# Kernel optimization log

Hardware: AMD Instinct MI355X
Metric: run time of the kernel (lower is better)

Reference implementation:

```python
import jax, jax.numpy as jnp
import numpy as np

D = 768      # hidden_size
H = 12       # num_head
HD = D // H  # head_dim
LN_EPS = 1e-5


def setup_inputs() -> dict:
    key = jax.random.key(0)
    ks = jax.random.split(key, 9)
    N, S = 4, 2048
    s = 0.02
    return {
        "hidden_state": jax.random.normal(ks[0], (N, S, D), dtype=jnp.float32),
        "key_padding_mask": jax.random.randint(ks[1], (N, S), 0, 2, dtype=jnp.int64),
        "Wq": jax.random.normal(ks[2], (D, D), dtype=jnp.float32) * s,
        "Wk": jax.random.normal(ks[3], (D, D), dtype=jnp.float32) * s,
        "Wv": jax.random.normal(ks[4], (D, D), dtype=jnp.float32) * s,
        "Wo": jax.random.normal(ks[5], (D, D), dtype=jnp.float32) * s,
        "W1": jax.random.normal(ks[6], (4 * D, D), dtype=jnp.float32) * s,
        "W2": jax.random.normal(ks[7], (D, 4 * D), dtype=jnp.float32) * s,
        "ln_g": jnp.ones((D,), dtype=jnp.float32),
        "ln_b": jnp.zeros((D,), dtype=jnp.float32),
    }


def _layernorm(x, g, b):
    mu = jnp.mean(x, axis=-1, keepdims=True)
    var = jnp.mean(jnp.square(x - mu), axis=-1, keepdims=True)
    return (x - mu) * jax.lax.rsqrt(var + LN_EPS) * g + b


def reference(hidden_state, key_padding_mask, Wq, Wk, Wv, Wo, W1, W2, ln_g, ln_b):
    x = hidden_state
    N, S, _ = x.shape
    # Note: original module projects K and V from `query` (self-attention).
    def proj(W):
        return (x @ W.T).reshape(N, S, H, HD).transpose(0, 2, 1, 3)  # [N,H,S,HD]
    Q, K, V = proj(Wq), proj(Wk), proj(Wv)
    scores = jnp.einsum("bhqd,bhkd->bhqk", Q, K)  # [N,H,S,S]
    # int mask: 0 marks padding positions -> masked with -inf
    pad = (key_padding_mask == 0)[:, None, None, :]  # [N,1,1,S]
    scores = jnp.where(pad, -jnp.inf, scores)
    attn = jax.nn.softmax(scores / np.sqrt(HD), axis=-1)
    ctx = jnp.einsum("bhqk,bhkd->bhqd", attn, V)
    ctx = ctx.transpose(0, 2, 1, 3).reshape(N, S, D)
    mha = ctx @ Wo.T
    # residual + LayerNorm (same LN params used twice, as in the original)
    n1 = _layernorm(x + mha, ln_g, ln_b)
    # FFN with exact GELU (torch nn.GELU default)
    f = jax.nn.gelu(n1 @ W1.T, approximate=False) @ W2.T
    return _layernorm(n1 + f, ln_g, ln_b)
```

## Files before the change

kernel.cpp:

```cpp
#include <hip/hip_runtime.h>
#include <math.h>

typedef unsigned short u16;
typedef unsigned int u32;
typedef __bf16 bf16x8 __attribute__((ext_vector_type(8)));
typedef float f32x4 __attribute__((ext_vector_type(4)));
typedef u32 u32x4 __attribute__((ext_vector_type(4)));

#define NB 4
#define SS 2048
#define DD 768
#define HH 12
#define HD 64
#define ROWS (NB*SS)

__device__ __forceinline__ u16 f2bf(float f) {
    union { float f; unsigned u; } v; v.f = f;
    unsigned r = v.u + 0x7fffu + ((v.u >> 16) & 1u);
    return (u16)(r >> 16);
}
__device__ __forceinline__ u32 fas(float f) { union { float f; u32 u; } v; v.f = f; return v.u; }

__device__ __forceinline__ void gl_lds16(const void* g, void* l) {
    __builtin_amdgcn_global_load_lds((__attribute__((address_space(1))) void*)(g),
                                     (__attribute__((address_space(3))) void*)(l),
                                     16, 0, 0);
}

__global__ __launch_bounds__(256) void prep_kernel(
        const float* __restrict__ X, const float* __restrict__ Wq,
        const float* __restrict__ Wk, const float* __restrict__ Wv,
        const float* __restrict__ Wo, const float* __restrict__ W1,
        const float* __restrict__ W2, const int* __restrict__ mask,
        u16* __restrict__ Xb, u16* __restrict__ Wqkvb, u16* __restrict__ Wob,
        u16* __restrict__ W1b, u16* __restrict__ W2b,
        int* __restrict__ cidx, int* __restrict__ cnt) {
    const int blk = blockIdx.x, tid = threadIdx.x;
    const float* src; u16* dst; int idx;
    if (blk < 6144)       { src = X;  dst = Xb;               idx = blk * 1024 + tid * 4; }
    else if (blk < 6720)  { src = Wq; dst = Wqkvb;            idx = (blk - 6144) * 1024 + tid * 4; }
    else if (blk < 7296)  { src = Wk; dst = Wqkvb + DD * DD;  idx = (blk - 6720) * 1024 + tid * 4; }
    else if (blk < 7872)  { src = Wv; dst = Wqkvb + 2*DD*DD;  idx = (blk - 7296) * 1024 + tid * 4; }
    else if (blk < 8448)  { src = Wo; dst = Wob;              idx = (blk - 7872) * 1024 + tid * 4; }
    else if (blk < 10752) { src = W1; dst = W1b;              idx = (blk - 8448) * 1024 + tid * 4; }
    else if (blk < 13056) { src = W2; dst = W2b;              idx = (blk - 10752) * 1024 + tid * 4; }
    else {
        const int b = blk - 13056;
        const int lane = tid & 63, wave = tid >> 6;
        const int base = b * SS + tid * 8;
        int4 m0 = *(const int4*)&mask[base];
        int4 m1 = *(const int4*)&mask[base + 4];
        int v[8] = { m0.x != 0, m0.y != 0, m0.z != 0, m0.w != 0,
                     m1.x != 0, m1.y != 0, m1.z != 0, m1.w != 0 };
        int own = 0;
#pragma unroll
        for (int i = 0; i < 8; ++i) own += v[i];
        int inc = own;
#pragma unroll
        for (int o = 1; o < 64; o <<= 1) {
            int n = __shfl_up(inc, o);
            if (lane >= o) inc += n;
        }
        __shared__ int wsum[4];
        if (lane == 63) wsum[wave] = inc;
        __syncthreads();
        int wbase = 0;
#pragma unroll
        for (int w = 0; w < 4; ++w) wbase += (w < wave) ? wsum[w] : 0;
        int pos = wbase + inc - own;
        int o8[8];
#pragma unroll
        for (int i = 0; i < 8; ++i) { o8[i] = v[i] ? pos : -1; pos += v[i]; }
        *(int4*)&cidx[base]     = make_int4(o8[0], o8[1], o8[2], o8[3]);
        *(int4*)&cidx[base + 4] = make_int4(o8[4], o8[5], o8[6], o8[7]);
        if (tid == 255) cnt[b] = wbase + inc;
        return;
    }
    float4 v = *(const float4*)&src[idx];
    ushort4 o;
    o.x = f2bf(v.x); o.y = f2bf(v.y); o.z = f2bf(v.z); o.w = f2bf(v.w);
    *(ushort4*)&dst[idx] = o;
}

template <int EPI, int BN>
__global__ __launch_bounds__(256) void gemm_bt(const u16* __restrict__ A,
                                               const u16* __restrict__ B,
                                               int M, int N, int K,
                                               void* __restrict__ out,
                                               const void* __restrict__ aux,
                                               u16* __restrict__ Qb,
                                               u16* __restrict__ Kb,
                                               u16* __restrict__ Vb,
                                               const int* __restrict__ cidx) {
    __shared__ __align__(16) u16 lA[2][128 * 64];
    __shared__ __align__(16) u16 lB[2][BN * 64];
    constexpr int MI = (BN == 128) ? 4 : 2;
    const int tid = threadIdx.x;
    const int lane = tid & 63, wave = tid >> 6;
    const int quad = lane >> 4, lc = lane & 15;
    const int xcd = blockIdx.x & 7, loc = blockIdx.x >> 3;
    const int mb = xcd * 8 + (loc & 7), nb = loc >> 3;
    const int m0 = mb * 128, n0 = nb * BN;
    const int wrow = (BN == 128) ? (wave >> 1) * 64 : wave * 32;
    const int wcol = (BN == 128) ? (wave & 1) * 64 : 0;
    const int swz = lc & 7;

    auto stage = [&](int bi, int kb) {
#pragma unroll
        for (int p0 = 0; p0 < 1024; p0 += 256) {
            int p = p0 + tid, row = p >> 3, cl = (p & 7) ^ (row & 7);
            gl_lds16(A + (size_t)(m0 + row) * K + kb + cl * 8, &lA[bi][(size_t)(p0 + wave * 64) * 8]);
        }
#pragma unroll
        for (int p0 = 0; p0 < BN * 8; p0 += 256) {
            int p = p0 + tid, row = p >> 3, cl = (p & 7) ^ (row & 7);
            gl_lds16(B + (size_t)(n0 + row) * K + kb + cl * 8, &lB[bi][(size_t)(p0 + wave * 64) * 8]);
        }
    };

    f32x4 acc[MI][4] = {};
    const int KT = K >> 6;

    stage(0, 0);
    for (int t = 0; t < KT; ++t) {
        const int cur = t & 1;
        if (t < KT - 1) {
            stage(cur ^ 1, (t + 1) << 6);
            __builtin_amdgcn_sched_barrier(0);
            if constexpr (BN == 128) asm volatile("s_waitcnt vmcnt(8)" ::: "memory");
            else                     asm volatile("s_waitcnt vmcnt(6)" ::: "memory");
        } else {
            __builtin_amdgcn_sched_barrier(0);
            asm volatile("s_waitcnt vmcnt(0)" ::: "memory");
        }
        __builtin_amdgcn_sched_barrier(0);
        __builtin_amdgcn_s_barrier();
        __builtin_amdgcn_sched_barrier(0);

        const u16* bA = &lA[cur][0];
        const u16* bB = &lB[cur][0];
#pragma unroll
        for (int k2 = 0; k2 < 2; ++k2) {
            bf16x8 af[MI], bfr[4];
#pragma unroll
            for (int t_ = 0; t_ < MI; ++t_)
                af[t_] = *(const bf16x8*)&bA[(wrow + t_ * 16 + lc) * 64 + ((quad + k2 * 4) ^ swz) * 8];
#pragma unroll
            for (int t_ = 0; t_ < 4; ++t_)
                bfr[t_] = *(const bf16x8*)&bB[(wcol + t_ * 16 + lc) * 64 + ((quad + k2 * 4) ^ swz) * 8];
            __builtin_amdgcn_s_setprio(1);
#pragma unroll
            for (int mi = 0; mi < MI; ++mi)
#pragma unroll
                for (int ni = 0; ni < 4; ++ni)
                    acc[mi][ni] = __builtin_amdgcn_mfma_f32_16x16x32_bf16(af[mi], bfr[ni],
                                                                         acc[mi][ni], 0, 0, 0);
            __builtin_amdgcn_s_setprio(0);
        }
        __builtin_amdgcn_sched_barrier(0);
        __builtin_amdgcn_s_barrier();
    }

#pragma unroll
    for (int mi = 0; mi < MI; ++mi) {
        int csa[4];
        if constexpr (EPI == 0) {
            int mbase = m0 + wrow + mi * 16 + quad * 4;
            int4 cs4 = *(const int4*)&cidx[(mbase >> 11) * SS + (mbase & 2047)];
            csa[0] = cs4.x; csa[1] = cs4.y; csa[2] = cs4.z; csa[3] = cs4.w;
        }
#pragma unroll
        for (int r = 0; r < 4; ++r) {
            int m = m0 + wrow + mi * 16 + quad * 4 + r;
#pragma unroll
            for (int ni = 0; ni < 4; ++ni) {
                int n = n0 + wcol + ni * 16 + lc;
                float v = acc[mi][ni][r];
                if constexpr (EPI == 0) {
                    int b = m >> 11, s = m & 2047;
                    int which = n / DD, rem = n - which * DD;
                    int h = rem >> 6, d = rem & 63;
                    u16* dst = which == 0 ? Qb : (which == 1 ? Kb : Vb);
                    int sidx = which == 0 ? s : csa[r];
                    if (sidx >= 0)
                        dst[((((size_t)b * HH + h) * SS + sidx) << 6) + d] = f2bf(v);
                } else if constexpr (EPI == 1) {
                    float u = v * fmaf(v * v, 0.035677408f, 0.7978845608f);
                    float e = __builtin_amdgcn_exp2f(u * 2.885390082f);
                    float g = v - v * __builtin_amdgcn_rcpf(e + 1.0f);
                    ((u16*)out)[(size_t)m * N + n] = f2bf(g);
                } else if constexpr (EPI == 2) {
                    ((float*)out)[(size_t)m * N + n] =
                        v + ((const float*)aux)[(size_t)m * N + n];
                } else {
                    ((float*)out)[(size_t)m * N + n] =
                        v + (float)(((const __bf16*)aux)[(size_t)m * N + n]);
                }
            }
        }
    }
}

__global__ __launch_bounds__(256) void transpose_v(const u16* __restrict__ V,
                                                   u16* __restrict__ Vt,
                                                   const int* __restrict__ cnt) {
    __shared__ u16 t[32][33];
    int bh = blockIdx.z;
    int c = cnt[bh / HH];
    int cr = (c + 63) & ~63;
    int s0 = blockIdx.x * 32, d0 = blockIdx.y * 32;
    if (s0 >= cr) return;
    const u16* vb = V + (size_t)bh * SS * HD;
    u16* vtb = Vt + (size_t)bh * HD * SS;
    int tx = threadIdx.x & 31, ty = threadIdx.x >> 5;
#pragma unroll
    for (int i = 0; i < 32; i += 8) {
        int s = s0 + ty + i;
        t[ty + i][tx] = (s < c) ? vb[(size_t)s * HD + d0 + tx] : (u16)0;
    }
    __syncthreads();
#pragma unroll
    for (int i = 0; i < 32; i += 8) vtb[(size_t)(d0 + ty + i) * SS + s0 + tx] = t[tx][ty + i];
}

__global__ __launch_bounds__(256, 3) void attn_kernel(const u16* __restrict__ Q,
                                                      const u16* __restrict__ K,
                                                      const u16* __restrict__ Vt,
                                                      const int* __restrict__ cntg,
                                                      u16* __restrict__ Ctx) {
    __shared__ __align__(16) u16 lK[2][4096];
    __shared__ __align__(16) u16 lV[2][4096];
    const int tid = threadIdx.x, lane = tid & 63, wave = tid >> 6;
    const int quad = lane >> 4, lc = lane & 15;
    const int bh = blockIdx.x % (NB * HH);
    const int b = bh / HH, h = bh - b * HH;
    const int q0 = (blockIdx.x / (NB * HH)) * 128;
    const u16* Qg = Q + ((size_t)bh * SS + q0 + wave * 32) * HD;
    const u16* Kg = K + (size_t)bh * SS * HD;
    const u16* Vg = Vt + (size_t)bh * HD * SS;
    const int sw = lc & 7;
    const int cnt = cntg[b];
    const int nt = (cnt + 63) >> 6;

    const int srow = tid >> 3, scl = (tid & 7) ^ (srow & 7);
    const int srow2 = (256 + tid) >> 3, scl2 = (tid & 7) ^ (srow2 & 7);

    auto stage = [&](int bi, int j0) {
        gl_lds16(Kg + (size_t)(j0 + srow) * HD + scl * 8,   &lK[bi][(size_t)(wave * 64) * 8]);
        gl_lds16(Kg + (size_t)(j0 + srow2) * HD + scl2 * 8, &lK[bi][(size_t)(256 + wave * 64) * 8]);
        gl_lds16(Vg + (size_t)srow * SS + j0 + scl * 8,     &lV[bi][(size_t)(wave * 64) * 8]);
        gl_lds16(Vg + (size_t)srow2 * SS + j0 + scl2 * 8,   &lV[bi][(size_t)(256 + wave * 64) * 8]);
    };

    bf16x8 qf[2][2];
#pragma unroll
    for (int mi = 0; mi < 2; ++mi)
#pragma unroll
        for (int k2 = 0; k2 < 2; ++k2)
            qf[mi][k2] = *(const bf16x8*)(Qg + (size_t)(mi * 16 + lc) * HD + k2 * 32 + quad * 8);

    bf16x8 onesf;
#pragma unroll
    for (int i = 0; i < 8; ++i) onesf[i] = (__bf16)1.0f;

    f32x4 oacc[2][4] = {};
    f32x4 lsum[2] = {};

    stage(0, 0);
    for (int t = 0; t < nt; ++t) {
        const int cur = t & 1;
        if (t < nt - 1) {
            stage(cur ^ 1, (t + 1) * 64);
            __builtin_amdgcn_sched_barrier(0);
            asm volatile("s_waitcnt vmcnt(4)" ::: "memory");
        } else {
            __builtin_amdgcn_sched_barrier(0);
            asm volatile("s_waitcnt vmcnt(0)" ::: "memory");
        }
        __builtin_amdgcn_sched_barrier(0);
        __builtin_amdgcn_s_barrier();
        __builtin_amdgcn_sched_barrier(0);

        const u16* bK = &lK[cur][0];
        const u16* bV = &lV[cur][0];

        f32x4 sacc[2][4] = {};
        __builtin_amdgcn_s_setprio(1);
#pragma unroll
        for (int k2 = 0; k2 < 2; ++k2) {
            bf16x8 kf[4];
#pragma unroll
            for (int ni = 0; ni < 4; ++ni)
                kf[ni] = *(const bf16x8*)&bK[(ni * 16 + lc) * 64 + ((quad + k2 * 4) ^ sw) * 8];
#pragma unroll
            for (int ni = 0; ni < 4; ++ni) {
                sacc[0][ni] = __builtin_amdgcn_mfma_f32_16x16x32_bf16(kf[ni], qf[0][k2], sacc[0][ni], 0, 0, 0);
                sacc[1][ni] = __builtin_amdgcn_mfma_f32_16x16x32_bf16(kf[ni], qf[1][k2], sacc[1][ni], 0, 0, 0);
            }
        }
        __builtin_amdgcn_s_setprio(0);

        const int kb_ = cnt - t * 64;
        const bool part = kb_ < 64;
        u32 pa[2][4], pb[2][4];
#pragma unroll
        for (int ni = 0; ni < 4; ++ni) {
#pragma unroll
            for (int mi = 0; mi < 2; ++mi) {
#pragma unroll
                for (int r = 0; r < 4; ++r) {
                    float e = __builtin_amdgcn_exp2f(sacc[mi][ni][r] * 0.180336880f);
                    if (part) e = (ni * 16 + quad * 4 + r < kb_) ? e : 0.0f;
                    sacc[mi][ni][r] = e;
                }
                pa[mi][ni] = __builtin_amdgcn_perm(fas(sacc[mi][ni][1]), fas(sacc[mi][ni][0]), 0x07060302);
                pb[mi][ni] = __builtin_amdgcn_perm(fas(sacc[mi][ni][3]), fas(sacc[mi][ni][2]), 0x07060302);
            }
        }

        bf16x8 pf[2][2];
#pragma unroll
        for (int mi = 0; mi < 2; ++mi)
#pragma unroll
            for (int k2 = 0; k2 < 2; ++k2) {
                u32 xa = pa[mi][2 * k2], ya = pa[mi][2 * k2 + 1];
                u32 xb = pb[mi][2 * k2], yb = pb[mi][2 * k2 + 1];
                asm("v_permlane32_swap_b32 %0, %1" : "+v"(xa), "+v"(ya));
                asm("v_permlane16_swap_b32 %0, %1" : "+v"(xa), "+v"(ya));
                asm("v_permlane32_swap_b32 %0, %1" : "+v"(xb), "+v"(yb));
                asm("v_permlane16_swap_b32 %0, %1" : "+v"(xb), "+v"(yb));
                u32x4 pw = { xa, xb, ya, yb };
                pf[mi][k2] = __builtin_bit_cast(bf16x8, pw);
            }

        __builtin_amdgcn_s_setprio(1);
#pragma unroll
        for (int k2 = 0; k2 < 2; ++k2) {
            lsum[0] = __builtin_amdgcn_mfma_f32_16x16x32_bf16(pf[0][k2], onesf, lsum[0], 0, 0, 0);
            lsum[1] = __builtin_amdgcn_mfma_f32_16x16x32_bf16(pf[1][k2], onesf, lsum[1], 0, 0, 0);
#pragma unroll
            for (int ni = 0; ni < 4; ++ni) {
                bf16x8 vf = *(const bf16x8*)&bV[(ni * 16 + lc) * 64 + ((quad + k2 * 4) ^ sw) * 8];
                oacc[0][ni] = __builtin_amdgcn_mfma_f32_16x16x32_bf16(pf[0][k2], vf, oacc[0][ni], 0, 0, 0);
                oacc[1][ni] = __builtin_amdgcn_mfma_f32_16x16x32_bf16(pf[1][k2], vf, oacc[1][ni], 0, 0, 0);
            }
        }
        __builtin_amdgcn_s_setprio(0);

        __builtin_amdgcn_sched_barrier(0);
        __builtin_amdgcn_s_barrier();
    }

#pragma unroll
    for (int mi = 0; mi < 2; ++mi)
#pragma unroll
        for (int r = 0; r < 4; ++r) {
            float inv = 1.0f / lsum[mi][r];
            int s = q0 + wave * 32 + mi * 16 + quad * 4 + r;
            size_t base = ((size_t)(b * SS + s)) * DD + h * HD;
#pragma unroll
            for (int ni = 0; ni < 4; ++ni)
                Ctx[base + ni * 16 + lc] = f2bf(oacc[mi][ni][r] * inv);
        }
}

__global__ __launch_bounds__(256) void ln_kernel(const float* __restrict__ in,
                                                 const float* __restrict__ g,
                                                 const float* __restrict__ bb,
                                                 u16* __restrict__ out_bf,
                                                 float* __restrict__ out_f) {
    const int row = blockIdx.x, tid = threadIdx.x;
    const float* x = in + (size_t)row * DD;
    float v0 = x[tid], v1 = x[tid + 256], v2 = x[tid + 512];
    float s = v0 + v1 + v2;
    float q = v0 * v0 + v1 * v1 + v2 * v2;
#pragma unroll
    for (int o = 1; o < 64; o <<= 1) {
        s += __shfl_xor(s, o);
        q += __shfl_xor(q, o);
    }
    __shared__ float rs[4], rq[4];
    int wave = tid >> 6;
    if ((tid & 63) == 0) { rs[wave] = s; rq[wave] = q; }
    __syncthreads();
    s = rs[0] + rs[1] + rs[2] + rs[3];
    q = rq[0] + rq[1] + rq[2] + rq[3];
    float mu = s * (1.0f / DD);
    float var = q * (1.0f / DD) - mu * mu;
    float rstd = rsqrtf(var + 1e-5f);
#pragma unroll
    for (int j = 0; j < 3; ++j) {
        int col = tid + j * 256;
        float v = (j == 0 ? v0 : (j == 1 ? v1 : v2));
        float y = (v - mu) * rstd * g[col] + bb[col];
        if (out_bf) out_bf[(size_t)row * DD + col] = f2bf(y);
        if (out_f) out_f[(size_t)row * DD + col] = y;
    }
}

extern "C" void kernel_launch(void* const* d_in, const int* in_sizes, int n_in,
                              void* d_out, int out_size, void* d_ws, size_t ws_size,
                              hipStream_t stream) {
    const float* X    = (const float*)d_in[0];
    const int*   mask = (const int*)d_in[1];
    const float* Wq   = (const float*)d_in[2];
    const float* Wk   = (const float*)d_in[3];
    const float* Wv   = (const float*)d_in[4];
    const float* Wo   = (const float*)d_in[5];
    const float* W1   = (const float*)d_in[6];
    const float* W2   = (const float*)d_in[7];
    const float* ln_g = (const float*)d_in[8];
    const float* ln_b = (const float*)d_in[9];
    float* out = (float*)d_out;

    char* ws = (char*)d_ws;
    size_t off = 0;
    auto alloc = [&](size_t bytes) {
        void* p = ws + off;
        off += (bytes + 255) & ~(size_t)255;
        return p;
    };
    u16*   Xbf   = (u16*)alloc((size_t)ROWS * DD * 2);
    u16*   Wqkvb = (u16*)alloc((size_t)3 * DD * DD * 2);
    u16*   Wob   = (u16*)alloc((size_t)DD * DD * 2);
    u16*   W1b   = (u16*)alloc((size_t)4 * DD * DD * 2);
    u16*   W2b   = (u16*)alloc((size_t)4 * DD * DD * 2);
    int*   cidx  = (int*)alloc((size_t)NB * SS * 4);
    int*   cnt   = (int*)alloc(256);
    u16*   Qb    = (u16*)alloc((size_t)ROWS * DD * 2);
    u16*   Kb    = (u16*)alloc((size_t)ROWS * DD * 2);
    u16*   Vb    = (u16*)alloc((size_t)ROWS * DD * 2);
    u16*   Vtb   = (u16*)alloc((size_t)ROWS * DD * 2);
    float* resid = (float*)alloc((size_t)ROWS * DD * 4);
    u16*   n1b   = (u16*)alloc((size_t)ROWS * DD * 2);
    u16*   Gb    = Qb;
    u16*   Ctxb  = Xbf;
    float* h2    = resid;

    prep_kernel<<<dim3(13056 + NB), dim3(256), 0, stream>>>(
        X, Wq, Wk, Wv, Wo, W1, W2, mask,
        Xbf, Wqkvb, Wob, W1b, W2b, cidx, cnt);

    gemm_bt<0, 128><<<dim3((3 * DD / 128) * (ROWS / 128)), dim3(256), 0, stream>>>(
        Xbf, Wqkvb, ROWS, 3 * DD, DD, nullptr, nullptr, Qb, Kb, Vb, cidx);

    transpose_v<<<dim3(SS / 32, HD / 32, NB * HH), dim3(256), 0, stream>>>(Vb, Vtb, cnt);

    attn_kernel<<<dim3((SS / 128) * (NB * HH)), dim3(256), 0, stream>>>(
        Qb, Kb, Vtb, cnt, Ctxb);

    gemm_bt<2, 64><<<dim3((DD / 64) * (ROWS / 128)), dim3(256), 0, stream>>>(
        Ctxb, Wob, ROWS, DD, DD, resid, X, nullptr, nullptr, nullptr, nullptr);

    ln_kernel<<<dim3(ROWS), dim3(256), 0, stream>>>(resid, ln_g, ln_b, n1b, nullptr);

    gemm_bt<1, 128><<<dim3((4 * DD / 128) * (ROWS / 128)), dim3(256), 0, stream>>>(
        n1b, W1b, ROWS, 4 * DD, DD, Gb, nullptr, nullptr, nullptr, nullptr, nullptr);

    gemm_bt<3, 64><<<dim3((DD / 64) * (ROWS / 128)), dim3(256), 0, stream>>>(
        Gb, W2b, ROWS, DD, 4 * DD, h2, n1b, nullptr, nullptr, nullptr, nullptr);

    ln_kernel<<<dim3(ROWS), dim3(256), 0, stream>>>(h2, ln_g, ln_b, nullptr, out);
}
```

Before: 345.5 us.

## Add 256x256 eight-wave GEMM for FFN up-projection and simplify generic GEMM loop

Adds a new 512-thread GEMM kernel with 256x256 output tiles, double-buffered LDS and interleaved prefetch of A and B halves between MFMA phases, used for the W1 GEMM with the GELU epilogue. The larger tile raises arithmetic intensity and reuse of each staged tile. Separately, the generic gemm_bt kernel loses its double buffering and priority hints and becomes a single-buffer load/sync/compute loop, which likely exposes global load latency in the QKV, Wo and W2 GEMMs. The new kernel uses 128KB of LDS per block and a large accumulator count, which may limit occupancy.

```diff
diff --git a/kernel.cpp b/kernel.cpp
--- a/kernel.cpp
+++ b/kernel.cpp
@@ -92,8 +92,8 @@
                                                u16* __restrict__ Kb,
                                                u16* __restrict__ Vb,
                                                const int* __restrict__ cidx) {
-    __shared__ __align__(16) u16 lA[2][128 * 64];
-    __shared__ __align__(16) u16 lB[2][BN * 64];
+    __shared__ __align__(16) u16 lA[128 * 64];
+    __shared__ __align__(16) u16 lB[BN * 64];
     constexpr int MI = (BN == 128) ? 4 : 2;
     const int tid = threadIdx.x;
     const int lane = tid & 63, wave = tid >> 6;
@@ -105,60 +105,37 @@
     const int wcol = (BN == 128) ? (wave & 1) * 64 : 0;
     const int swz = lc & 7;
 
-    auto stage = [&](int bi, int kb) {
+    f32x4 acc[MI][4] = {};
+
+    for (int kb = 0; kb < K; kb += 64) {
+        __syncthreads();
 #pragma unroll
         for (int p0 = 0; p0 < 1024; p0 += 256) {
             int p = p0 + tid, row = p >> 3, cl = (p & 7) ^ (row & 7);
-            gl_lds16(A + (size_t)(m0 + row) * K + kb + cl * 8, &lA[bi][(size_t)(p0 + wave * 64) * 8]);
+            gl_lds16(A + (size_t)(m0 + row) * K + kb + cl * 8, &lA[(size_t)(p0 + wave * 64) * 8]);
         }
 #pragma unroll
         for (int p0 = 0; p0 < BN * 8; p0 += 256) {
             int p = p0 + tid, row = p >> 3, cl = (p & 7) ^ (row & 7);
-            gl_lds16(B + (size_t)(n0 + row) * K + kb + cl * 8, &lB[bi][(size_t)(p0 + wave * 64) * 8]);
-        }
-    };
-
-    f32x4 acc[MI][4] = {};
-    const int KT = K >> 6;
-
-    stage(0, 0);
-    for (int t = 0; t < KT; ++t) {
-        const int cur = t & 1;
-        if (t < KT - 1) {
-            stage(cur ^ 1, (t + 1) << 6);
-            __builtin_amdgcn_sched_barrier(0);
-            if constexpr (BN == 128) asm volatile("s_waitcnt vmcnt(8)" ::: "memory");
-            else                     asm volatile("s_waitcnt vmcnt(6)" ::: "memory");
-        } else {
-            __builtin_amdgcn_sched_barrier(0);
-            asm volatile("s_waitcnt vmcnt(0)" ::: "memory");
-        }
-        __builtin_amdgcn_sched_barrier(0);
-        __builtin_amdgcn_s_barrier();
-        __builtin_amdgcn_sched_barrier(0);
-
-        const u16* bA = &lA[cur][0];
-        const u16* bB = &lB[cur][0];
+            gl_lds16(B + (size_t)(n0 + row) * K + kb + cl * 8, &lB[(size_t)(p0 + wave * 64) * 8]);
+        }
+        __syncthreads();
 #pragma unroll
         for (int k2 = 0; k2 < 2; ++k2) {
             bf16x8 af[MI], bfr[4];
 #pragma unroll
-            for (int t_ = 0; t_ < MI; ++t_)
-                af[t_] = *(const bf16x8*)&bA[(wrow + t_ * 16 + lc) * 64 + ((quad + k2 * 4) ^ swz) * 8];
-#pragma unroll
-            for (int t_ = 0; t_ < 4; ++t_)
-                bfr[t_] = *(const bf16x8*)&bB[(wcol + t_ * 16 + lc) * 64 + ((quad + k2 * 4) ^ swz) * 8];
-            __builtin_amdgcn_s_setprio(1);
+            for (int t = 0; t < MI; ++t)
+                af[t] = *(const bf16x8*)&lA[(wrow + t * 16 + lc) * 64 + ((quad + k2 * 4) ^ swz) * 8];
+#pragma unroll
+            for (int t = 0; t < 4; ++t)
+                bfr[t] = *(const bf16x8*)&lB[(wcol + t * 16 + lc) * 64 + ((quad + k2 * 4) ^ swz) * 8];
 #pragma unroll
             for (int mi = 0; mi < MI; ++mi)
 #pragma unroll
                 for (int ni = 0; ni < 4; ++ni)
                     acc[mi][ni] = __builtin_amdgcn_mfma_f32_16x16x32_bf16(af[mi], bfr[ni],
                                                                          acc[mi][ni], 0, 0, 0);
-            __builtin_amdgcn_s_setprio(0);
-        }
-        __builtin_amdgcn_sched_barrier(0);
-        __builtin_amdgcn_s_barrier();
+        }
     }
 
 #pragma unroll
@@ -201,6 +178,158 @@
     }
 }
 
+template <int EPI>
+__global__ __launch_bounds__(512, 2) void gemm256_bt(const u16* __restrict__ A,
+                                                     const u16* __restrict__ B,
+                                                     int M, int N, int K,
+                                                     void* __restrict__ out) {
+    __shared__ __align__(16) u16 lA[2][256 * 64];
+    __shared__ __align__(16) u16 lB[2][256 * 64];
+    const int tid = threadIdx.x;
+    const int lane = tid & 63, wave = tid >> 6;
+    const int quad = lane >> 4, lc = lane & 15;
+    const int xcd = blockIdx.x & 7, loc = blockIdx.x >> 3;
+    const int mpx = (M >> 8) >> 3;
+    const int mb = xcd * mpx + (loc % mpx), nb = loc / mpx;
+    const int m0 = mb * 256, n0 = nb * 256;
+    const int wrow = (wave >> 2) * 128;
+    const int wcol = (wave & 3) * 64;
+    const int swz = lc & 7;
+
+    auto stageA = [&](int bi, int kb, int r) {
+        int p = r * 512 + tid, row = p >> 3, cl = (p & 7) ^ (row & 7);
+        gl_lds16(A + (size_t)(m0 + row) * K + kb + cl * 8,
+                 &lA[bi][(size_t)(r * 512 + wave * 64) * 8]);
+    };
+    auto stageB = [&](int bi, int kb, int r) {
+        int p = r * 512 + tid, row = p >> 3, cl = (p & 7) ^ (row & 7);
+        gl_lds16(B + (size_t)(n0 + row) * K + kb + cl * 8,
+                 &lB[bi][(size_t)(r * 512 + wave * 64) * 8]);
+    };
+
+    f32x4 acc[8][4] = {};
+    const int KT = K >> 6;
+
+#pragma unroll
+    for (int r = 0; r < 4; ++r) stageA(0, 0, r);
+#pragma unroll
+    for (int r = 0; r < 4; ++r) stageB(0, 0, r);
+    asm volatile("s_waitcnt vmcnt(0)" ::: "memory");
+    __builtin_amdgcn_sched_barrier(0);
+    __builtin_amdgcn_s_barrier();
+    __builtin_amdgcn_sched_barrier(0);
+
+    for (int t = 0; t < KT; ++t) {
+        const int cur = t & 1;
+        const u16* bA = &lA[cur][0];
+        const u16* bB = &lB[cur][0];
+        const bool pf = (t + 1) < KT;
+        const int kb1 = (t + 1) << 6;
+        bf16x8 af[4], bf[4];
+
+#pragma unroll
+        for (int i = 0; i < 4; ++i)
+            af[i] = *(const bf16x8*)&bA[(wrow + i * 16 + lc) * 64 + (quad ^ swz) * 8];
+#pragma unroll
+        for (int j = 0; j < 4; ++j)
+            bf[j] = *(const bf16x8*)&bB[(wcol + j * 16 + lc) * 64 + (quad ^ swz) * 8];
+        if (pf) { stageA(cur ^ 1, kb1, 0); stageA(cur ^ 1, kb1, 1);
+                  stageA(cur ^ 1, kb1, 2); stageA(cur ^ 1, kb1, 3); }
+        __builtin_amdgcn_sched_barrier(0);
+        __builtin_amdgcn_s_barrier();
+        asm volatile("s_waitcnt lgkmcnt(0)" ::: "memory");
+        __builtin_amdgcn_sched_barrier(0);
+        __builtin_amdgcn_s_setprio(1);
+#pragma unroll
+        for (int i = 0; i < 4; ++i)
+#pragma unroll
+            for (int j = 0; j < 4; ++j)
+                acc[i][j] = __builtin_amdgcn_mfma_f32_16x16x32_bf16(af[i], bf[j], acc[i][j], 0, 0, 0);
+        __builtin_amdgcn_s_setprio(0);
+        __builtin_amdgcn_sched_barrier(0);
+        __builtin_amdgcn_s_barrier();
+        __builtin_amdgcn_sched_barrier(0);
+
+#pragma unroll
+        for (int i = 0; i < 4; ++i)
+            af[i] = *(const bf16x8*)&bA[(wrow + 64 + i * 16 + lc) * 64 + (quad ^ swz) * 8];
+        if (pf) { stageB(cur ^ 1, kb1, 0); stageB(cur ^ 1, kb1, 1);
+                  stageB(cur ^ 1, kb1, 2); stageB(cur ^ 1, kb1, 3); }
+        __builtin_amdgcn_sched_barrier(0);
+        __builtin_amdgcn_s_barrier();
+        asm volatile("s_waitcnt lgkmcnt(0)" ::: "memory");
+        __builtin_amdgcn_sched_barrier(0);
+        __builtin_amdgcn_s_setprio(1);
+#pragma unroll
+        for (int i = 0; i < 4; ++i)
+#pragma unroll
+            for (int j = 0; j < 4; ++j)
+                acc[4 + i][j] = __builtin_amdgcn_mfma_f32_16x16x32_bf16(af[i], bf[j], acc[4 + i][j], 0, 0, 0);
+        __builtin_amdgcn_s_setprio(0);
+        __builtin_amdgcn_sched_barrier(0);
+        __builtin_amdgcn_s_barrier();
+        __builtin_amdgcn_sched_barrier(0);
+
+#pragma unroll
+        for (int i = 0; i < 4; ++i)
+            af[i] = *(const bf16x8*)&bA[(wrow + i * 16 + lc) * 64 + ((quad + 4) ^ swz) * 8];
+#pragma unroll
+        for (int j = 0; j < 4; ++j)
+            bf[j] = *(const bf16x8*)&bB[(wcol + j * 16 + lc) * 64 + ((quad + 4) ^ swz) * 8];
+        __builtin_amdgcn_sched_barrier(0);
+        __builtin_amdgcn_s_barrier();
+        asm volatile("s_waitcnt lgkmcnt(0)" ::: "memory");
+        __builtin_amdgcn_sched_barrier(0);
+        __builtin_amdgcn_s_setprio(1);
+#pragma unroll
+        for (int i = 0; i < 4; ++i)
+#pragma unroll
+            for (int j = 0; j < 4; ++j)
+                acc[i][j] = __builtin_amdgcn_mfma_f32_16x16x32_bf16(af[i], bf[j], acc[i][j], 0, 0, 0);
+        __builtin_amdgcn_s_setprio(0);
+        __builtin_amdgcn_sched_barrier(0);
+        __builtin_amdgcn_s_barrier();
+        __builtin_amdgcn_sched_barrier(0);
+
+#pragma unroll
+        for (int i = 0; i < 4; ++i)
+            af[i] = *(const bf16x8*)&bA[(wrow + 64 + i * 16 + lc) * 64 + ((quad + 4) ^ swz) * 8];
+        __builtin_amdgcn_sched_barrier(0);
+        __builtin_amdgcn_s_barrier();
+        asm volatile("s_waitcnt lgkmcnt(0)" ::: "memory");
+        __builtin_amdgcn_sched_barrier(0);
+        __builtin_amdgcn_s_setprio(1);
+#pragma unroll
+        for (int i = 0; i < 4; ++i)
+#pragma unroll
+            for (int j = 0; j < 4; ++j)
+                acc[4 + i][j] = __builtin_amdgcn_mfma_f32_16x16x32_bf16(af[i], bf[j], acc[4 + i][j], 0, 0, 0);
+        __builtin_amdgcn_s_setprio(0);
+        if (pf) asm volatile("s_waitcnt vmcnt(0)" ::: "memory");
+        __builtin_amdgcn_sched_barrier(0);
+        __builtin_amdgcn_s_barrier();
+        __builtin_amdgcn_sched_barrier(0);
+    }
+
+#pragma unroll
+    for (int mi = 0; mi < 8; ++mi) {
+        int mrow = m0 + wrow + (mi >> 2) * 64 + (mi & 3) * 16 + quad * 4;
+#pragma unroll
+        for (int r = 0; r < 4; ++r) {
+            int m = mrow + r;
+#pragma unroll
+            for (int ni = 0; ni < 4; ++ni) {
+                int n = n0 + wcol + ni * 16 + lc;
+                float v = acc[mi][ni][r];
+                float u = v * fmaf(v * v, 0.035677408f, 0.7978845608f);
+                float e = __builtin_amdgcn_exp2f(u * 2.885390082f);
+                float g = v - v * __builtin_amdgcn_rcpf(e + 1.0f);
+                ((u16*)out)[(size_t)m * N + n] = f2bf(g);
+            }
+        }
+    }
+}
+
 __global__ __launch_bounds__(256) void transpose_v(const u16* __restrict__ V,
                                                    u16* __restrict__ Vt,
                                                    const int* __restrict__ cnt) {
@@ -454,8 +583,8 @@
 
     ln_kernel<<<dim3(ROWS), dim3(256), 0, stream>>>(resid, ln_g, ln_b, n1b, nullptr);
 
-    gemm_bt<1, 128><<<dim3((4 * DD / 128) * (ROWS / 128)), dim3(256), 0, stream>>>(
-        n1b, W1b, ROWS, 4 * DD, DD, Gb, nullptr, nullptr, nullptr, nullptr, nullptr);
+    gemm256_bt<1><<<dim3((ROWS / 256) * (4 * DD / 256)), dim3(512), 0, stream>>>(
+        n1b, W1b, ROWS, 4 * DD, DD, Gb);
 
     gemm_bt<3, 64><<<dim3((DD / 64) * (ROWS / 128)), dim3(256), 0, stream>>>(
         Gb, W2b, ROWS, DD, 4 * DD, h2, n1b, nullptr, nullptr, nullptr, nullptr);
```

Measured after the change: 340.4 us. No clear change (-1.5%).
